# Kernel optimization log

Measured on AMD Instinct MI355X. Metric: run time of the kernel, lower is better.

## Reference

```python
import math
import jax, jax.numpy as jnp
import numpy as np

V, D, DEPTH, H, DH, FF = 32000, 1024, 4, 16, 64, 4096
B, N = 1, 2048


def setup_inputs() -> dict:
    key = jax.random.key(0)
    ks = jax.random.split(key, 8)
    s = 0.02
    return {
        "x": jax.random.randint(ks[0], (B, N), 0, V, dtype=jnp.int32),
        "token_emb": jax.random.normal(ks[1], (V, D), jnp.float32) * s,
        "attn_gamma": jnp.ones((DEPTH, D), jnp.float32),
        "w_qkv": jax.random.normal(ks[2], (DEPTH, D, 3 * H * DH), jnp.float32) * s,
        "w_attn_out": jax.random.normal(ks[3], (DEPTH, H * DH, D), jnp.float32) * s,
        "ff_gamma": jnp.ones((DEPTH, D), jnp.float32),
        "w_ff1": jax.random.normal(ks[4], (DEPTH, D, FF), jnp.float32) * s,
        "b_ff1": jnp.zeros((DEPTH, FF), jnp.float32),
        "w_ff2": jax.random.normal(ks[5], (DEPTH, FF, D), jnp.float32) * s,
        "b_ff2": jnp.zeros((DEPTH, D), jnp.float32),
        "final_gamma": jnp.ones((D,), jnp.float32),
        "w_logits": jax.random.normal(ks[6], (D, V), jnp.float32) * s,
    }


def rms_norm(x, gamma):
    # F.normalize(x, dim=-1) * sqrt(D) * gamma
    norm = jnp.sqrt(jnp.sum(x * x, axis=-1, keepdims=True))
    return x / jnp.maximum(norm, 1e-12) * (x.shape[-1] ** 0.5) * gamma


def rope_cos_sin(n, dh, dtype):
    # lucidrains rotary-embedding-torch default: interleaved pairs
    inv_freq = 1.0 / (10000.0 ** (jnp.arange(0, dh, 2, dtype=jnp.float32) / dh))
    freqs = jnp.arange(n, dtype=jnp.float32)[:, None] * inv_freq[None, :]  # [n, dh/2]
    freqs = jnp.repeat(freqs, 2, axis=-1)  # [n, dh]
    return jnp.cos(freqs).astype(dtype), jnp.sin(freqs).astype(dtype)


def rotate_half(x):
    x1 = x[..., 0::2]
    x2 = x[..., 1::2]
    return jnp.stack((-x2, x1), axis=-1).reshape(x.shape)


def apply_rope(t, cos, sin):
    # t: [b, h, n, dh]; cos/sin: [n, dh]
    return t * cos[None, None] + rotate_half(t) * sin[None, None]


def decoder_forward(x, token_emb, attn_gamma, w_qkv, w_attn_out, ff_gamma,
                    w_ff1, b_ff1, w_ff2, b_ff2, final_gamma, w_logits):
    b, n = x.shape
    h = token_emb[x]  # [b, n, D]
    cos, sin = rope_cos_sin(n, DH, h.dtype)
    causal = jnp.triu(jnp.ones((n, n), bool), k=1)
    scale = DH ** -0.5
    neg = -jnp.finfo(h.dtype).max
    for l in range(DEPTH):
        # attention block
        xn = rms_norm(h, attn_gamma[l])
        qkv = xn @ w_qkv[l]  # [b, n, 3*H*DH]
        qkv = qkv.reshape(b, n, 3, H, DH).transpose(2, 0, 3, 1, 4)  # [3, b, H, n, DH]
        q, k, v = qkv[0], qkv[1], qkv[2]
        q = apply_rope(q, cos, sin)
        k = apply_rope(k, cos, sin)
        sim = jnp.einsum('bhid,bhjd->bhij', q, k) * scale
        sim = jnp.where(causal, neg, sim)
        attn = jax.nn.softmax(sim, axis=-1)
        out = jnp.einsum('bhij,bhjd->bhid', attn, v)
        out = out.transpose(0, 2, 1, 3).reshape(b, n, H * DH) @ w_attn_out[l]
        h = h + out
        # feedforward block
        fn = rms_norm(h, ff_gamma[l])
        ff = jax.nn.gelu(fn @ w_ff1[l] + b_ff1[l], approximate=False) @ w_ff2[l] + b_ff2[l]
        h = h + ff
    return rms_norm(h, final_gamma) @ w_logits


def reference(x, token_emb, attn_gamma, w_qkv, w_attn_out, ff_gamma,
              w_ff1, b_ff1, w_ff2, b_ff2, final_gamma, w_logits):
    return decoder_forward(x, token_emb, attn_gamma, w_qkv, w_attn_out, ff_gamma,
                           w_ff1, b_ff1, w_ff2, b_ff2, final_gamma, w_logits)
```

## Files before the change

### kernel.cpp

```cpp
#include <hip/hip_runtime.h>
#include <math.h>


#define NSEQ 2048
#define DMODEL 1024
#define NH 16
#define DHEAD 64
#define FFD 4096
#define VOC 32000
#define NLAYER 4

typedef unsigned short u16;
typedef short bf16x8 __attribute__((ext_vector_type(8)));
typedef float f32x4 __attribute__((ext_vector_type(4)));

__device__ __forceinline__ u16 f2bf(float f) {
  unsigned int u = __builtin_bit_cast(unsigned int, f);
  u += 0x7fffu + ((u >> 16) & 1u);
  return (u16)(u >> 16);
}

__device__ __forceinline__ void gload16(const void* g, void* l) {
  __builtin_amdgcn_global_load_lds((__attribute__((address_space(1))) void*)g,
                                   (__attribute__((address_space(3))) void*)l,
                                   16, 0, 0);
}

__device__ __forceinline__ f32x4 mfma16x32(bf16x8 a, bf16x8 b, f32x4 c) {
  return __builtin_amdgcn_mfma_f32_16x16x32_bf16(a, b, c, 0, 0, 0);
}

template <int N>
__device__ __forceinline__ void waitvm() {
  if constexpr (N == 0) asm volatile("s_waitcnt vmcnt(0)" ::: "memory");
  else if constexpr (N == 2) asm volatile("s_waitcnt vmcnt(2)" ::: "memory");
  else if constexpr (N == 3) asm volatile("s_waitcnt vmcnt(3)" ::: "memory");
  else if constexpr (N == 4) asm volatile("s_waitcnt vmcnt(4)" ::: "memory");
  else if constexpr (N == 6) asm volatile("s_waitcnt vmcnt(6)" ::: "memory");
  else if constexpr (N == 8) asm volatile("s_waitcnt vmcnt(8)" ::: "memory");
}


__global__ __launch_bounds__(256) void k_embed(const int* __restrict__ x,
                                               const float* __restrict__ emb,
                                               float* __restrict__ h,
                                               float* __restrict__ ct,
                                               float* __restrict__ st) {
  const int n = blockIdx.x, t = threadIdx.x;
  const int tok = x[n];
  reinterpret_cast<float4*>(h + (size_t)n * DMODEL)[t] =
      reinterpret_cast<const float4*>(emb + (size_t)tok * DMODEL)[t];
  if (t < 32) {
    const double inv = exp(-(double)(2 * t) / 64.0 * log(10000.0));
    const double a = (double)n * inv;
    ct[n * 32 + t] = (float)cos(a);
    st[n * 32 + t] = (float)sin(a);
  }
}

__global__ __launch_bounds__(256) void k_transpose(const float* __restrict__ in0,
                                                   u16* __restrict__ out0,
                                                   int K, int Nc,
                                                   size_t ls_in, size_t ls_out) {
  const float* in = in0 + blockIdx.z * ls_in;
  u16* out = out0 + blockIdx.z * ls_out;
  __shared__ float tile[64][65];
  const int kb = blockIdx.x * 64, nb = blockIdx.y * 64;
  const int tr = threadIdx.x >> 4;
  const int tc = threadIdx.x & 15;
#pragma unroll
  for (int r = 0; r < 64; r += 16) {
    const float4 v = *reinterpret_cast<const float4*>(
        &in[(size_t)(kb + r + tr) * Nc + nb + tc * 4]);
    tile[r + tr][tc * 4 + 0] = v.x;
    tile[r + tr][tc * 4 + 1] = v.y;
    tile[r + tr][tc * 4 + 2] = v.z;
    tile[r + tr][tc * 4 + 3] = v.w;
  }
  __syncthreads();
#pragma unroll
  for (int r = 0; r < 64; r += 16) {
    const int n = r + tr;
    ushort4 o;
    o.x = f2bf(tile[tc * 4 + 0][n]);
    o.y = f2bf(tile[tc * 4 + 1][n]);
    o.z = f2bf(tile[tc * 4 + 2][n]);
    o.w = f2bf(tile[tc * 4 + 3][n]);
    const unsigned long long ull = __builtin_bit_cast(unsigned long long, o);
    __builtin_nontemporal_store(
        ull, reinterpret_cast<unsigned long long*>(
                 &out[(size_t)(nb + n) * K + kb + tc * 4]));
  }
}

__global__ __launch_bounds__(256) void k_rmsnorm(const float* __restrict__ h,
                                                 const float* __restrict__ gamma,
                                                 u16* __restrict__ out) {
  __shared__ float red[4];
  const int n = blockIdx.x, t = threadIdx.x;
  const float4 v = reinterpret_cast<const float4*>(h + (size_t)n * DMODEL)[t];
  float ss = v.x * v.x + v.y * v.y + v.z * v.z + v.w * v.w;
#pragma unroll
  for (int off = 32; off; off >>= 1) ss += __shfl_down(ss, off);
  if ((t & 63) == 0) red[t >> 6] = ss;
  __syncthreads();
  const float tot = red[0] + red[1] + red[2] + red[3];
  const float inv = 32.0f / fmaxf(sqrtf(tot), 1e-12f);
  const float4 g = reinterpret_cast<const float4*>(gamma)[t];
  ushort4 o;
  o.x = f2bf(v.x * inv * g.x);
  o.y = f2bf(v.y * inv * g.y);
  o.z = f2bf(v.z * inv * g.z);
  o.w = f2bf(v.w * inv * g.w);
  reinterpret_cast<ushort4*>(out + (size_t)n * DMODEL)[t] = o;
}

#define EPI_STORE 0
#define EPI_ADD 1
#define EPI_GELU 2
#define EPI_BIAS_ADD 3
#define EPI_QKV 4
#define EPI_ATOM 5

__device__ __forceinline__ bf16x8 ldsfragT(const char* base, int row, int lg) {
  return *reinterpret_cast<const bf16x8*>(
      base + row * 64 + (((lg ^ (row & 3) ^ ((row >> 2) & 3)) & 3) << 4));
}

template <int EPI, int BM, int BN, int KSPLIT>
__global__ __launch_bounds__(256) void k_gemmT(
    const u16* __restrict__ A, const u16* __restrict__ BT, int K, int Nc,
    int NMB, const float* __restrict__ bias, const float* __restrict__ add,
    float* __restrict__ outf, u16* __restrict__ outb,
    u16* __restrict__ Qr, u16* __restrict__ Kr, u16* __restrict__ VT,
    const float* __restrict__ ct, const float* __restrict__ st) {
  constexpr int MFR = BM / 32;
  constexpr int NFR = BN / 32;
  constexpr int ABYTES = BM * 64;
  constexpr int BBYTES = BN * 64;
  constexpr int BUFB = ABYTES + BBYTES;
  constexpr int SL = BM / 64 + BN / 64;
  __shared__ alignas(16) char sm[4 * BUFB];
  const int nt = K >> 5;
  int bid = blockIdx.x;
  int ksp = 0;
  int inner = gridDim.x;
  if constexpr (KSPLIT == 2) {
    inner = gridDim.x >> 1;
    ksp = bid / inner;
    bid = bid % inner;
  }
  int swz = bid;
  if ((inner & 7) == 0) swz = (swz & 7) * (inner >> 3) + (swz >> 3);
  const int mb = swz % NMB, nb = swz / NMB;
  const int m0 = mb * BM, n0 = nb * BN;
  const int lda = K * KSPLIT;
  const size_t kofs = (size_t)ksp * K;

  const int tid = threadIdx.x, w = tid >> 6, lane = tid & 63;
  const int wr = w >> 1, wc = w & 1;
  const int lr = lane & 15, lg = lane >> 4;

  const int srow = tid >> 2;
  const int gslot = (tid & 3) ^ (srow & 3) ^ ((srow >> 2) & 3);
  const u16* ga0 = A + (size_t)(m0 + srow) * lda + kofs + gslot * 8;
  const u16* ga1 = A + (size_t)(m0 + (BM == 128 ? 64 : 0) + srow) * lda + kofs + gslot * 8;
  const u16* gb0 = BT + (size_t)(n0 + srow) * lda + kofs + gslot * 8;
  const u16* gb1 = BT + (size_t)(n0 + (BN == 128 ? 64 : 0) + srow) * lda + kofs + gslot * 8;
  const int ldOff = tid * 16;

  auto stage = [&](int b) {
    char* base = sm + b * BUFB;
    gload16(ga0, base + ldOff);
    if constexpr (BM == 128) gload16(ga1, base + 4096 + ldOff);
    gload16(gb0, base + ABYTES + ldOff);
    if constexpr (BN == 128) gload16(gb1, base + ABYTES + 4096 + ldOff);
    ga0 += 32; gb0 += 32;
    if constexpr (BM == 128) ga1 += 32;
    if constexpr (BN == 128) gb1 += 32;
  };

  stage(0);
  stage(1);
  stage(2);
  waitvm<2 * SL>();
  __builtin_amdgcn_s_barrier();

  f32x4 acc[MFR][NFR] = {};
  int cur = 0;
  for (int t = 0; t < nt; ++t) {
    const char* Ab = sm + cur * BUFB;
    const char* Bb = Ab + ABYTES;
    bf16x8 af[MFR], bf[NFR];
#pragma unroll
    for (int i = 0; i < MFR; ++i)
      af[i] = ldsfragT(Ab, wr * (BM / 2) + i * 16 + lr, lg);
#pragma unroll
    for (int i = 0; i < NFR; ++i)
      bf[i] = ldsfragT(Bb, wc * (BN / 2) + i * 16 + lr, lg);
    if (t + 3 < nt) stage((cur + 3) & 3);
    __builtin_amdgcn_s_setprio(1);
#pragma unroll
    for (int mi = 0; mi < MFR; ++mi)
#pragma unroll
      for (int nj = 0; nj < NFR; ++nj)
        acc[mi][nj] = mfma16x32(af[mi], bf[nj], acc[mi][nj]);
    __builtin_amdgcn_s_setprio(0);
    if (t + 1 < nt) {
      __builtin_amdgcn_sched_barrier(0);
      if (t + 3 < nt)      waitvm<2 * SL>();
      else if (t + 2 < nt) waitvm<SL>();
      else                 waitvm<0>();
      __builtin_amdgcn_s_barrier();
      __builtin_amdgcn_sched_barrier(0);
    }
    cur = (cur + 1) & 3;
  }

  if constexpr (EPI == EPI_QKV) {
#pragma unroll
    for (int mi = 0; mi < MFR; ++mi) {
#pragma unroll
      for (int nj = 0; nj < NFR; ++nj) {
        const int col = n0 + wc * (BN / 2) + nj * 16 + lr;
        const int which = col >> 10;
        const int hh = (col >> 6) & 15;
        const int d = col & 63;
#pragma unroll
        for (int r = 0; r < 4; ++r) {
          const int row = m0 + wr * (BM / 2) + mi * 16 + lg * 4 + r;
          const float v = acc[mi][nj][r];
          if (which == 2) {
            VT[((size_t)hh * DHEAD + d) * NSEQ + row] = f2bf(v);
          } else {
            const float part = __shfl_xor(v, 1);
            const float sgn = (d & 1) ? 1.0f : -1.0f;
            const float c = ct[row * 32 + (d >> 1)];
            const float s_ = st[row * 32 + (d >> 1)];
            const u16 o = f2bf(v * c + sgn * part * s_);
            u16* dst = (which == 0) ? Qr : Kr;
            dst[((size_t)hh * NSEQ + row) * DHEAD + d] = o;
          }
        }
      }
    }
    return;
  }
#pragma unroll
  for (int mi = 0; mi < MFR; ++mi) {
#pragma unroll
    for (int nj = 0; nj < NFR; ++nj) {
      const int col = n0 + wc * (BN / 2) + nj * 16 + lr;
#pragma unroll
      for (int r = 0; r < 4; ++r) {
        const int row = m0 + wr * (BM / 2) + mi * 16 + lg * 4 + r;
        const size_t idx = (size_t)row * Nc + col;
        float v = acc[mi][nj][r];
        if (EPI == EPI_ATOM) {
          if (ksp == 0) v += bias[col];
          atomicAdd(&outf[idx], v);
        } else if (EPI == EPI_GELU) {
          v += bias[col];
          v = 0.5f * v * (1.0f + erff(v * 0.70710678118654752f));
          outb[idx] = f2bf(v);
        } else if (EPI == EPI_ADD) {
          outf[idx] = v + add[idx];
        } else if (EPI == EPI_BIAS_ADD) {
          outf[idx] = v + bias[col] + add[idx];
        } else {
          outf[idx] = v;
        }
      }
    }
  }
}

template <int EPI>
__global__ __launch_bounds__(256, 2) void k_gemmW(
    const u16* __restrict__ A, const u16* __restrict__ BT, int K, int Nc,
    const float* __restrict__ bias, float* __restrict__ outf,
    u16* __restrict__ outb) {
  constexpr int ABYTES = 8192;
  constexpr int BUFB = ABYTES + 16384;
  __shared__ alignas(16) char sm[3 * BUFB];
  const int nt = K >> 5;
  const int NMB = 16;
  const int nwg = gridDim.x;
  int swz = blockIdx.x;
  if ((nwg & 7) == 0) swz = (swz & 7) * (nwg >> 3) + (swz >> 3);
  const int mb = swz % NMB, nb = swz / NMB;
  const int m0 = mb * 128, n0 = nb * 256;

  const int tid = threadIdx.x, w = tid >> 6, lane = tid & 63;
  const int wr = w >> 1, wc = w & 1;
  const int lr = lane & 15, lg = lane >> 4;

  const int srow = tid >> 2;
  const int gslot = (tid & 3) ^ (srow & 3) ^ ((srow >> 2) & 3);
  const u16* ga0 = A + (size_t)(m0 + srow) * K + gslot * 8;
  const u16* ga1 = A + (size_t)(m0 + 64 + srow) * K + gslot * 8;
  const u16* gb0 = BT + (size_t)(n0 + srow) * K + gslot * 8;
  const u16* gb1 = BT + (size_t)(n0 + 64 + srow) * K + gslot * 8;
  const u16* gb2 = BT + (size_t)(n0 + 128 + srow) * K + gslot * 8;
  const u16* gb3 = BT + (size_t)(n0 + 192 + srow) * K + gslot * 8;
  const int ldOff = tid * 16;

  auto stage = [&](int b) {
    char* base = sm + b * BUFB;
    gload16(ga0, base + ldOff);
    gload16(ga1, base + 4096 + ldOff);
    gload16(gb0, base + ABYTES + ldOff);
    gload16(gb1, base + ABYTES + 4096 + ldOff);
    gload16(gb2, base + ABYTES + 8192 + ldOff);
    gload16(gb3, base + ABYTES + 12288 + ldOff);
    ga0 += 32; ga1 += 32; gb0 += 32; gb1 += 32; gb2 += 32; gb3 += 32;
  };

  stage(0);
  stage(1);
  waitvm<6>();
  __builtin_amdgcn_s_barrier();

  f32x4 acc[4][8] = {};
  int cur = 0, nx2 = 2;
  for (int t = 0; t < nt; ++t) {
    const char* Ab = sm + cur * BUFB;
    const char* Bb = Ab + ABYTES;
    const bool pf = (t + 2 < nt);
    bf16x8 af[4], bf[8];
#pragma unroll
    for (int i = 0; i < 4; ++i)
      af[i] = ldsfragT(Ab, wr * 64 + i * 16 + lr, lg);
#pragma unroll
    for (int i = 0; i < 8; ++i)
      bf[i] = ldsfragT(Bb, wc * 128 + i * 16 + lr, lg);
    if (pf) stage(nx2);
    __builtin_amdgcn_s_setprio(1);
#pragma unroll
    for (int mi = 0; mi < 4; ++mi)
#pragma unroll
      for (int nj = 0; nj < 8; ++nj)
        acc[mi][nj] = mfma16x32(af[mi], bf[nj], acc[mi][nj]);
    __builtin_amdgcn_s_setprio(0);
    if (t + 1 < nt) {
      __builtin_amdgcn_sched_barrier(0);
      if (pf) waitvm<6>();
      else    waitvm<0>();
      __builtin_amdgcn_s_barrier();
      __builtin_amdgcn_sched_barrier(0);
    }
    cur = (cur == 2) ? 0 : cur + 1;
    nx2 = (nx2 == 2) ? 0 : nx2 + 1;
  }

#pragma unroll
  for (int mi = 0; mi < 4; ++mi) {
#pragma unroll
    for (int nj = 0; nj < 8; ++nj) {
      const int col = n0 + wc * 128 + nj * 16 + lr;
#pragma unroll
      for (int r = 0; r < 4; ++r) {
        const int row = m0 + wr * 64 + mi * 16 + lg * 4 + r;
        const size_t idx = (size_t)row * Nc + col;
        float v = acc[mi][nj][r];
        if (EPI == EPI_GELU) {
          v += bias[col];
          v = 0.5f * v * (1.0f + erff(v * 0.70710678118654752f));
          outb[idx] = f2bf(v);
        } else {
          outf[idx] = v;
        }
      }
    }
  }
}

__global__ __launch_bounds__(256) void k_attn(const u16* __restrict__ Qr,
                                              const u16* __restrict__ Kr,
                                              const u16* __restrict__ VT,
                                              u16* __restrict__ O) {
  __shared__ alignas(16) u16 Pl[4][16 * 32];
  const int id = blockIdx.x;
  int qb, hh;
  if (id < 256) { qb = id & 31; hh = id >> 5; }
  else          { qb = 31 - (id & 31); hh = 8 + ((id - 256) >> 5); }
  const int w = threadIdx.x >> 6, lane = threadIdx.x & 63;
  const int lr = lane & 15, lg = lane >> 4;
  const int q0 = qb * 64 + w * 16;
  const u16* Qh = Qr + (size_t)hh * NSEQ * DHEAD;
  const u16* Kh = Kr + (size_t)hh * NSEQ * DHEAD;
  const u16* Vh = VT + (size_t)hh * DHEAD * NSEQ;
  u16* Pw = Pl[w];

  const bf16x8 aq0 = *reinterpret_cast<const bf16x8*>(Qh + (q0 + lr) * DHEAD + lg * 8);
  const bf16x8 aq1 = *reinterpret_cast<const bf16x8*>(Qh + (q0 + lr) * DHEAD + 32 + lg * 8);

  f32x4 o0 = {}, o1 = {}, o2 = {}, o3 = {};
  float m[4], l[4];
#pragma unroll
  for (int r = 0; r < 4; ++r) { m[r] = -1e30f; l[r] = 0.0f; }

  const int jend = q0 + 15;

  auto loadK = [&](int j0, bf16x8* bk) {
    bk[0] = *reinterpret_cast<const bf16x8*>(Kh + (j0 + lr) * DHEAD + lg * 8);
    bk[1] = *reinterpret_cast<const bf16x8*>(Kh + (j0 + lr) * DHEAD + 32 + lg * 8);
    bk[2] = *reinterpret_cast<const bf16x8*>(Kh + (j0 + 16 + lr) * DHEAD + lg * 8);
    bk[3] = *reinterpret_cast<const bf16x8*>(Kh + (j0 + 16 + lr) * DHEAD + 32 + lg * 8);
  };
  auto loadV = [&](int j0, bf16x8* vv) {
    const u16* vb = Vh + j0 + lg * 8;
    vv[0] = *reinterpret_cast<const bf16x8*>(vb + (0 + lr) * NSEQ);
    vv[1] = *reinterpret_cast<const bf16x8*>(vb + (16 + lr) * NSEQ);
    vv[2] = *reinterpret_cast<const bf16x8*>(vb + (32 + lr) * NSEQ);
    vv[3] = *reinterpret_cast<const bf16x8*>(vb + (48 + lr) * NSEQ);
  };

  bf16x8 bk[4], vv[4], bkN[4], vvN[4];
  loadK(0, bk);
  loadV(0, vv);

  for (int j0 = 0; j0 <= jend; j0 += 32) {
    if (j0 + 32 <= jend) { loadK(j0 + 32, bkN); loadV(j0 + 32, vvN); }

    f32x4 s0 = {}, s1 = {};
    s0 = mfma16x32(aq0, bk[0], s0);
    s0 = mfma16x32(aq1, bk[1], s0);
    s1 = mfma16x32(aq0, bk[2], s1);
    s1 = mfma16x32(aq1, bk[3], s1);

    float sv0[4], sv1[4], pm[4];
#pragma unroll
    for (int r = 0; r < 4; ++r) {
      const int irow = q0 + lg * 4 + r;
      sv0[r] = (j0 + lr > irow) ? -1e30f : s0[r] * 0.125f;
      sv1[r] = (j0 + 16 + lr > irow) ? -1e30f : s1[r] * 0.125f;
      pm[r] = fmaxf(sv0[r], sv1[r]);
    }
#pragma unroll
    for (int off = 1; off < 16; off <<= 1)
#pragma unroll
      for (int r = 0; r < 4; ++r) pm[r] = fmaxf(pm[r], __shfl_xor(pm[r], off));
    float p0[4], p1[4], rs[4];
    f32x4 fv;
#pragma unroll
    for (int r = 0; r < 4; ++r) {
      const float mn = fmaxf(m[r], pm[r]);
      fv[r] = __expf(m[r] - mn);
      m[r] = mn;
      p0[r] = __expf(sv0[r] - mn);
      p1[r] = __expf(sv1[r] - mn);
      rs[r] = p0[r] + p1[r];
    }
#pragma unroll
    for (int off = 1; off < 16; off <<= 1)
#pragma unroll
      for (int r = 0; r < 4; ++r) rs[r] += __shfl_xor(rs[r], off);
#pragma unroll
    for (int r = 0; r < 4; ++r) l[r] = l[r] * fv[r] + rs[r];
    o0 *= fv; o1 *= fv; o2 *= fv; o3 *= fv;

#pragma unroll
    for (int r = 0; r < 4; ++r) {
      Pw[(lg * 4 + r) * 32 + lr] = f2bf(p0[r]);
      Pw[(lg * 4 + r) * 32 + 16 + lr] = f2bf(p1[r]);
    }
    const bf16x8 pa = *reinterpret_cast<const bf16x8*>(Pw + lr * 32 + lg * 8);
    o0 = mfma16x32(pa, vv[0], o0);
    o1 = mfma16x32(pa, vv[1], o1);
    o2 = mfma16x32(pa, vv[2], o2);
    o3 = mfma16x32(pa, vv[3], o3);

#pragma unroll
    for (int i = 0; i < 4; ++i) { bk[i] = bkN[i]; vv[i] = vvN[i]; }
  }

#pragma unroll
  for (int r = 0; r < 4; ++r) {
    const int row = q0 + lg * 4 + r;
    const float invl = 1.0f / l[r];
    u16* orow = O + (size_t)row * DMODEL + hh * DHEAD;
    orow[0 * 16 + lr] = f2bf(o0[r] * invl);
    orow[1 * 16 + lr] = f2bf(o1[r] * invl);
    orow[2 * 16 + lr] = f2bf(o2[r] * invl);
    orow[3 * 16 + lr] = f2bf(o3[r] * invl);
  }
}


extern "C" void kernel_launch(void* const* d_in, const int* in_sizes, int n_in,
                              void* d_out, int out_size, void* d_ws, size_t ws_size,
                              hipStream_t stream) {
  (void)in_sizes; (void)n_in;
  const int* x = (const int*)d_in[0];
  const float* emb = (const float*)d_in[1];
  const float* attn_gamma = (const float*)d_in[2];
  const float* w_qkv = (const float*)d_in[3];
  const float* w_attn_out = (const float*)d_in[4];
  const float* ff_gamma = (const float*)d_in[5];
  const float* w_ff1 = (const float*)d_in[6];
  const float* b_ff1 = (const float*)d_in[7];
  const float* w_ff2 = (const float*)d_in[8];
  const float* b_ff2 = (const float*)d_in[9];
  const float* final_gamma = (const float*)d_in[10];
  const float* w_logits = (const float*)d_in[11];
  float* out = (float*)d_out;

  const size_t EARLY_NEED = 176ull << 20;
  const size_t FINAL_NEED = 72ull << 20;
  char* earlyBase;
  char* finalBase;
  if (ws_size >= EARLY_NEED + FINAL_NEED) {
    earlyBase = (char*)d_ws;
    finalBase = (char*)d_ws + EARLY_NEED;
  } else if (ws_size >= FINAL_NEED && (size_t)out_size * 4 >= EARLY_NEED) {
    earlyBase = (char*)d_out;
    finalBase = (char*)d_ws;
  } else {
    return;
  }
  size_t eoff = 0, foff = 0;
  auto ealloc = [&](size_t b) { void* p = earlyBase + eoff; eoff += (b + 255) & ~(size_t)255; return p; };
  auto falloc = [&](size_t b) { void* p = finalBase + foff; foff += (b + 255) & ~(size_t)255; return p; };

  u16* wqkvT = (u16*)ealloc((size_t)NLAYER * 3072 * DMODEL * 2);
  u16* wattnT = (u16*)ealloc((size_t)NLAYER * DMODEL * DMODEL * 2);
  u16* wff1T = (u16*)ealloc((size_t)NLAYER * FFD * DMODEL * 2);
  u16* wff2T = (u16*)ealloc((size_t)NLAYER * DMODEL * FFD * 2);
  float* h = (float*)ealloc((size_t)NSEQ * DMODEL * 4);
  u16* Qr = (u16*)ealloc((size_t)NH * NSEQ * DHEAD * 2);
  u16* Kr = (u16*)ealloc((size_t)NH * NSEQ * DHEAD * 2);
  u16* VTb = (u16*)ealloc((size_t)NH * NSEQ * DHEAD * 2);
  u16* Ob = (u16*)ealloc((size_t)NSEQ * DMODEL * 2);
  u16* ff1b = (u16*)ealloc((size_t)NSEQ * FFD * 2);
  float* ct = (float*)ealloc((size_t)NSEQ * 32 * 4);
  float* st = (float*)ealloc((size_t)NSEQ * 32 * 4);
  u16* wlogT = (u16*)falloc((size_t)VOC * DMODEL * 2);
  u16* xn = (u16*)falloc((size_t)NSEQ * DMODEL * 2);

  k_embed<<<dim3(NSEQ), 256, 0, stream>>>(x, emb, h, ct, st);
  k_transpose<<<dim3(16, 48, NLAYER), 256, 0, stream>>>(
      w_qkv, wqkvT, DMODEL, 3072, (size_t)DMODEL * 3072, (size_t)3072 * DMODEL);
  k_transpose<<<dim3(16, 16, NLAYER), 256, 0, stream>>>(
      w_attn_out, wattnT, DMODEL, DMODEL, (size_t)DMODEL * DMODEL, (size_t)DMODEL * DMODEL);
  k_transpose<<<dim3(16, 64, NLAYER), 256, 0, stream>>>(
      w_ff1, wff1T, DMODEL, FFD, (size_t)DMODEL * FFD, (size_t)FFD * DMODEL);
  k_transpose<<<dim3(64, 16, NLAYER), 256, 0, stream>>>(
      w_ff2, wff2T, FFD, DMODEL, (size_t)FFD * DMODEL, (size_t)DMODEL * FFD);
  k_transpose<<<dim3(16, 500, 1), 256, 0, stream>>>(
      w_logits, wlogT, DMODEL, VOC, 0, 0);

  for (int lyr = 0; lyr < NLAYER; ++lyr) {
    k_rmsnorm<<<dim3(NSEQ), 256, 0, stream>>>(h, attn_gamma + (size_t)lyr * DMODEL, xn);
    k_gemmT<EPI_QKV, 64, 128, 1><<<dim3(32 * 24), 256, 0, stream>>>(
        xn, wqkvT + (size_t)lyr * 3072 * DMODEL, DMODEL, 3072, 32,
        nullptr, nullptr, nullptr, nullptr, Qr, Kr, VTb, ct, st);
    k_attn<<<dim3(512), 256, 0, stream>>>(Qr, Kr, VTb, Ob);
    k_gemmT<EPI_ADD, 64, 64, 1><<<dim3(32 * 16), 256, 0, stream>>>(
        Ob, wattnT + (size_t)lyr * DMODEL * DMODEL, DMODEL, DMODEL, 32,
        nullptr, h, h, nullptr, nullptr, nullptr, nullptr, nullptr, nullptr);
    k_rmsnorm<<<dim3(NSEQ), 256, 0, stream>>>(h, ff_gamma + (size_t)lyr * DMODEL, xn);
    k_gemmT<EPI_GELU, 64, 128, 1><<<dim3(32 * 32), 256, 0, stream>>>(
        xn, wff1T + (size_t)lyr * FFD * DMODEL, DMODEL, FFD, 32,
        b_ff1 + (size_t)lyr * FFD, nullptr, nullptr, ff1b,
        nullptr, nullptr, nullptr, nullptr, nullptr);
    k_gemmT<EPI_ATOM, 64, 64, 2><<<dim3(32 * 16 * 2), 256, 0, stream>>>(
        ff1b, wff2T + (size_t)lyr * DMODEL * FFD, FFD / 2, DMODEL, 32,
        b_ff2 + (size_t)lyr * DMODEL, nullptr, h, nullptr,
        nullptr, nullptr, nullptr, nullptr, nullptr);
  }

  k_rmsnorm<<<dim3(NSEQ), 256, 0, stream>>>(h, final_gamma, xn);
  k_gemmW<EPI_STORE><<<dim3(16 * 125), 256, 0, stream>>>(
      xn, wlogT, DMODEL, VOC, nullptr, out, nullptr);
}
```

Measured before the change: 1.199 ms.

## Use 256x256 tile with 8 waves and 4-stage pipeline for logits GEMM

Measured after the change: 1.200 ms. No clear change (+0.1%).

```diff
diff --git a/kernel.cpp b/kernel.cpp
--- a/kernel.cpp
+++ b/kernel.cpp
@@ -275,101 +275,88 @@
   }
 }
 
-template <int EPI>
-__global__ __launch_bounds__(256, 2) void k_gemmW(
+__global__ __launch_bounds__(512, 2) void k_gemm256(
     const u16* __restrict__ A, const u16* __restrict__ BT, int K, int Nc,
-    const float* __restrict__ bias, float* __restrict__ outf,
-    u16* __restrict__ outb) {
-  constexpr int ABYTES = 8192;
-  constexpr int BUFB = ABYTES + 16384;
-  __shared__ alignas(16) char sm[3 * BUFB];
+    float* __restrict__ outf) {
+  constexpr int ABYTES = 256 * 64;
+  constexpr int BUFB = 2 * ABYTES;
+  constexpr int SL = 4;
+  __shared__ alignas(16) char sm[4 * BUFB];
   const int nt = K >> 5;
-  const int NMB = 16;
+  const int NMB = 8;
   const int nwg = gridDim.x;
   int swz = blockIdx.x;
   if ((nwg & 7) == 0) swz = (swz & 7) * (nwg >> 3) + (swz >> 3);
   const int mb = swz % NMB, nb = swz / NMB;
-  const int m0 = mb * 128, n0 = nb * 256;
+  const int m0 = mb * 256, n0 = nb * 256;
 
   const int tid = threadIdx.x, w = tid >> 6, lane = tid & 63;
-  const int wr = w >> 1, wc = w & 1;
+  const int wr = w >> 2, wc = w & 3;
   const int lr = lane & 15, lg = lane >> 4;
 
   const int srow = tid >> 2;
   const int gslot = (tid & 3) ^ (srow & 3) ^ ((srow >> 2) & 3);
   const u16* ga0 = A + (size_t)(m0 + srow) * K + gslot * 8;
-  const u16* ga1 = A + (size_t)(m0 + 64 + srow) * K + gslot * 8;
+  const u16* ga1 = A + (size_t)(m0 + 128 + srow) * K + gslot * 8;
   const u16* gb0 = BT + (size_t)(n0 + srow) * K + gslot * 8;
-  const u16* gb1 = BT + (size_t)(n0 + 64 + srow) * K + gslot * 8;
-  const u16* gb2 = BT + (size_t)(n0 + 128 + srow) * K + gslot * 8;
-  const u16* gb3 = BT + (size_t)(n0 + 192 + srow) * K + gslot * 8;
+  const u16* gb1 = BT + (size_t)(n0 + 128 + srow) * K + gslot * 8;
   const int ldOff = tid * 16;
 
   auto stage = [&](int b) {
     char* base = sm + b * BUFB;
     gload16(ga0, base + ldOff);
-    gload16(ga1, base + 4096 + ldOff);
+    gload16(ga1, base + 8192 + ldOff);
     gload16(gb0, base + ABYTES + ldOff);
-    gload16(gb1, base + ABYTES + 4096 + ldOff);
-    gload16(gb2, base + ABYTES + 8192 + ldOff);
-    gload16(gb3, base + ABYTES + 12288 + ldOff);
-    ga0 += 32; ga1 += 32; gb0 += 32; gb1 += 32; gb2 += 32; gb3 += 32;
+    gload16(gb1, base + ABYTES + 8192 + ldOff);
+    ga0 += 32; ga1 += 32; gb0 += 32; gb1 += 32;
   };
 
   stage(0);
   stage(1);
-  waitvm<6>();
+  stage(2);
+  waitvm<2 * SL>();
   __builtin_amdgcn_s_barrier();
 
-  f32x4 acc[4][8] = {};
-  int cur = 0, nx2 = 2;
+  f32x4 acc[8][4] = {};
+  int cur = 0;
   for (int t = 0; t < nt; ++t) {
     const char* Ab = sm + cur * BUFB;
     const char* Bb = Ab + ABYTES;
-    const bool pf = (t + 2 < nt);
-    bf16x8 af[4], bf[8];
+    bf16x8 af[8], bf[4];
+#pragma unroll
+    for (int i = 0; i < 8; ++i)
+      af[i] = ldsfragT(Ab, wr * 128 + i * 16 + lr, lg);
 #pragma unroll
     for (int i = 0; i < 4; ++i)
-      af[i] = ldsfragT(Ab, wr * 64 + i * 16 + lr, lg);
-#pragma unroll
-    for (int i = 0; i < 8; ++i)
-      bf[i] = ldsfragT(Bb, wc * 128 + i * 16 + lr, lg);
-    if (pf) stage(nx2);
+      bf[i] = ldsfragT(Bb, wc * 64 + i * 16 + lr, lg);
+    if (t + 3 < nt) stage((cur + 3) & 3);
     __builtin_amdgcn_s_setprio(1);
 #pragma unroll
-    for (int mi = 0; mi < 4; ++mi)
-#pragma unroll
-      for (int nj = 0; nj < 8; ++nj)
+    for (int mi = 0; mi < 8; ++mi)
+#pragma unroll
+      for (int nj = 0; nj < 4; ++nj)
         acc[mi][nj] = mfma16x32(af[mi], bf[nj], acc[mi][nj]);
     __builtin_amdgcn_s_setprio(0);
     if (t + 1 < nt) {
       __builtin_amdgcn_sched_barrier(0);
-      if (pf) waitvm<6>();
-      else    waitvm<0>();
+      if (t + 3 < nt)      waitvm<2 * SL>();
+      else if (t + 2 < nt) waitvm<SL>();
+      else                 waitvm<0>();
       __builtin_amdgcn_s_barrier();
       __builtin_amdgcn_sched_barrier(0);
     }
-    cur = (cur == 2) ? 0 : cur + 1;
-    nx2 = (nx2 == 2) ? 0 : nx2 + 1;
-  }
-
-#pragma unroll
-  for (int mi = 0; mi < 4; ++mi) {
-#pragma unroll
-    for (int nj = 0; nj < 8; ++nj) {
-      const int col = n0 + wc * 128 + nj * 16 + lr;
+    cur = (cur + 1) & 3;
+  }
+
+#pragma unroll
+  for (int mi = 0; mi < 8; ++mi) {
+#pragma unroll
+    for (int nj = 0; nj < 4; ++nj) {
+      const int col = n0 + wc * 64 + nj * 16 + lr;
 #pragma unroll
       for (int r = 0; r < 4; ++r) {
-        const int row = m0 + wr * 64 + mi * 16 + lg * 4 + r;
-        const size_t idx = (size_t)row * Nc + col;
-        float v = acc[mi][nj][r];
-        if (EPI == EPI_GELU) {
-          v += bias[col];
-          v = 0.5f * v * (1.0f + erff(v * 0.70710678118654752f));
-          outb[idx] = f2bf(v);
-        } else {
-          outf[idx] = v;
-        }
+        const int row = m0 + wr * 128 + mi * 16 + lg * 4 + r;
+        outf[(size_t)row * Nc + col] = acc[mi][nj][r];
       }
     }
   }
@@ -571,6 +558,5 @@
   }
 
   k_rmsnorm<<<dim3(NSEQ), 256, 0, stream>>>(h, final_gamma, xn);
-  k_gemmW<EPI_STORE><<<dim3(16 * 125), 256, 0, stream>>>(
-      xn, wlogT, DMODEL, VOC, nullptr, out, nullptr);
-}
+  k_gemm256<<<dim3(8 * 125), 512, 0, stream>>>(xn, wlogT, DMODEL, VOC, out);
+}
```
